# Performance work log

Hardware: AMD Instinct MI355X
Metric: run time of the kernel (lower is better)

## Reference

```python
import jax, jax.numpy as jnp
import numpy as np

N, F, H = 512, 256, 512

def _w(k, i, o):
    return jax.random.normal(k, (i, o), jnp.float32) * (1.0 / np.sqrt(i))

def setup_inputs() -> dict:
    key = jax.random.key(0)
    ks = jax.random.split(key, 12)
    z = lambda n: jnp.zeros((n,), jnp.float32)
    return {
        "node_features": jax.random.normal(ks[0], (N, F), jnp.float32),
        "adjacency": jax.random.uniform(ks[1], (N, N), jnp.float32),
        # GraphConv layers: neighbor linear (wl,bl) and self-loop (ws,bs)
        "gc1_wl": _w(ks[2], F, H), "gc1_bl": z(H), "gc1_ws": _w(ks[3], F, H), "gc1_bs": z(H),
        "gc2_wl": _w(ks[4], H, H), "gc2_bl": z(H), "gc2_ws": _w(ks[5], H, H), "gc2_bs": z(H),
        "gc3_wl": _w(ks[6], H, F), "gc3_bl": z(F), "gc3_ws": _w(ks[7], H, F), "gc3_bs": z(F),
        # edge MLP: Linear(2F,H) -> ReLU -> (dropout=identity, eval) -> Linear(H,H) -> ReLU -> Linear(H,1)
        "mlp_w1": _w(ks[8], 2 * F, H), "mlp_b1": z(H),
        "mlp_w2": _w(ks[9], H, H), "mlp_b2": z(H),
        "mlp_w3": _w(ks[10], H, 1), "mlp_b3": z(1),
    }

def _gconv(x, adj_norm, wl, bl, ws, bs):
    # adj_norm @ Linear(x) + SelfLoop(x)
    return adj_norm @ (x @ wl + bl) + (x @ ws + bs)

def reference(node_features, adjacency,
              gc1_wl, gc1_bl, gc1_ws, gc1_bs,
              gc2_wl, gc2_bl, gc2_ws, gc2_bs,
              gc3_wl, gc3_bl, gc3_ws, gc3_bs,
              mlp_w1, mlp_b1, mlp_w2, mlp_b2, mlp_w3, mlp_b3):
    # row-normalized adjacency (shared across all three layers)
    adj_norm = adjacency / (adjacency.sum(axis=1, keepdims=True) + 1e-8)
    x = jax.nn.relu(_gconv(node_features, adj_norm, gc1_wl, gc1_bl, gc1_ws, gc1_bs))
    x = jax.nn.relu(_gconv(x, adj_norm, gc2_wl, gc2_bl, gc2_ws, gc2_bs))
    emb = _gconv(x, adj_norm, gc3_wl, gc3_bl, gc3_ws, gc3_bs)  # [N, F]
    # vectorized all-pairs (i<j) edge scoring, symmetric scatter
    iu, ju = np.triu_indices(N, k=1)  # static index lists, P = N(N-1)/2
    ef = jnp.concatenate([emb[iu], emb[ju]], axis=-1)  # [P, 2F]
    h = jax.nn.relu(ef @ mlp_w1 + mlp_b1)
    h = jax.nn.relu(h @ mlp_w2 + mlp_b2)
    s = jax.nn.sigmoid((h @ mlp_w3 + mlp_b3)[:, 0])  # [P]
    edge_scores = jnp.zeros((N, N), emb.dtype).at[iu, ju].set(s).at[ju, iu].set(s)
    return emb, edge_scores
```

## Files before the change

### kernel.cpp

```cpp
#include <hip/hip_runtime.h>
#include <hip/hip_bf16.h>


#define NN 512
#define FF 256
#define HH 512

typedef __attribute__((ext_vector_type(8))) short s8v;
typedef __attribute__((ext_vector_type(4))) float f4v;

__device__ __forceinline__ ushort f2bf(float f) {
  unsigned u = __float_as_uint(f);
  unsigned r = (u + 0x7fffu + ((u >> 16) & 1u)) >> 16;
  return (ushort)r;
}

__global__ __launch_bounds__(256)
void prep_kernel(const float* __restrict__ adj, float* __restrict__ adjn,
                 const float* __restrict__ w2, ushort* __restrict__ w2t2) {
  int b = blockIdx.x;
  int tid = threadIdx.x;
  if (b < 512) {
    const float* r = adj + b * NN;
    float a0 = r[tid], a1 = r[tid + 256];
    float s = a0 + a1;
#pragma unroll
    for (int m = 1; m < 64; m <<= 1) s += __shfl_xor(s, m);
    __shared__ float wsum[4];
    if ((tid & 63) == 0) wsum[tid >> 6] = s;
    __syncthreads();
    float inv = 1.f / (wsum[0] + wsum[1] + wsum[2] + wsum[3] + 1e-8f);
    float* o = adjn + b * NN;
    o[tid] = a0 * inv;
    o[tid + 256] = a1 * inv;
  } else {
    int b2 = b - 512;
    int slab = b2 >> 3;
    int col = (b2 & 7) * 64 + (tid >> 2);
    int kq = tid & 3;
    int k0 = slab * 32 + kq * 8;
    ushort tmp[8];
#pragma unroll
    for (int e = 0; e < 8; ++e) tmp[e] = f2bf(w2[(k0 + e) * HH + col]);
    ushort* dst = w2t2 + slab * 16384 + col * 32 + kq * 8;
    *(ushort4*)dst = *(ushort4*)tmp;
    *(ushort4*)(dst + 4) = *(ushort4*)&tmp[4];
  }
}

template <bool RELU>
__global__ __launch_bounds__(256)
void gemm_ts(int M, int N, int K,
             const float* __restrict__ A, int lda,
             const float* __restrict__ B0, const float* __restrict__ B1, int ldb,
             const float* __restrict__ bias0, const float* __restrict__ bias1,
             const float* __restrict__ add0, const float* __restrict__ add1, int ldadd,
             float* __restrict__ C0, float* __restrict__ C1, int ldc)
{
  const float* B = blockIdx.z ? B1 : B0;
  const float* bias = blockIdx.z ? bias1 : bias0;
  const float* add = blockIdx.z ? add1 : add0;
  float* C = blockIdx.z ? C1 : C0;
  const int n0 = blockIdx.x * 64;
  const int m0 = blockIdx.y * 16;
  const int tid = threadIdx.x;
  const int ty = tid >> 4, tx = tid & 15;

  __shared__ float As[32][18];
  __shared__ float Bs[32][68];
  float4 acc = {0.f, 0.f, 0.f, 0.f};

  const int am = tid >> 4;
  const int ak = tid & 15;
  const int bk = tid >> 4;
  const int bn = tid & 15;

  float2 pa = *(const float2*)&A[(m0 + am) * lda + ak * 2];
  float4 pb0 = *(const float4*)&B[bk * ldb + n0 + bn * 4];
  float4 pb1 = *(const float4*)&B[(bk + 16) * ldb + n0 + bn * 4];

  for (int k0 = 0; k0 < K; k0 += 32) {
    As[ak * 2][am] = pa.x;
    As[ak * 2 + 1][am] = pa.y;
    *(float4*)&Bs[bk][bn * 4] = pb0;
    *(float4*)&Bs[bk + 16][bn * 4] = pb1;
    __syncthreads();
    if (k0 + 32 < K) {
      pa = *(const float2*)&A[(m0 + am) * lda + k0 + 32 + ak * 2];
      pb0 = *(const float4*)&B[(k0 + 32 + bk) * ldb + n0 + bn * 4];
      pb1 = *(const float4*)&B[(k0 + 48 + bk) * ldb + n0 + bn * 4];
    }
#pragma unroll
    for (int k = 0; k < 32; ++k) {
      float a = As[k][ty];
      float4 b = *(const float4*)&Bs[k][tx * 4];
      acc.x += a * b.x; acc.y += a * b.y; acc.z += a * b.z; acc.w += a * b.w;
    }
    __syncthreads();
  }

  int m = m0 + ty;
  float4 v = acc;
  if (bias) {
    float4 bv = *(const float4*)&bias[n0 + tx * 4];
    v.x += bv.x; v.y += bv.y; v.z += bv.z; v.w += bv.w;
  }
  if (add) {
    float4 d = *(const float4*)&add[m * ldadd + n0 + tx * 4];
    v.x += d.x; v.y += d.y; v.z += d.z; v.w += d.w;
  }
  if (RELU) {
    v.x = fmaxf(v.x, 0.f); v.y = fmaxf(v.y, 0.f);
    v.z = fmaxf(v.z, 0.f); v.w = fmaxf(v.w, 0.f);
  }
  *(float4*)&C[m * ldc + n0 + tx * 4] = v;
}

__global__ __launch_bounds__(512)
__attribute__((amdgpu_waves_per_eu(2, 2)))
void edge_mlp(const float* __restrict__ Amat, const float* __restrict__ Bmat,
              const ushort* __restrict__ w2t2,
              const float* __restrict__ b2, const float* __restrict__ w3,
              const float* __restrict__ b3,
              float* __restrict__ edges)
{
  __shared__ ushort h1s[2][128 * 128];
  __shared__ float part[8][640];

  const int tb = (int)blockIdx.x;
  int bj = (int)((sqrtf(4.f * tb + 1.f) - 1.f) * 0.5f);
  while (bj * bj + bj > tb) --bj;
  while ((bj + 1) * (bj + 2) <= tb) ++bj;
  const int bi = tb - bj * bj - bj;

  const int tid = threadIdx.x;
  const int wid = tid >> 6;
  const int lane = tid & 63;
  const int l15 = lane & 15;
  const int lg = lane >> 4;

  const f4v zero = {0.f, 0.f, 0.f, 0.f};
  f4v acc[8][4];
#pragma unroll
  for (int mf = 0; mf < 8; ++mf)
#pragma unroll
    for (int nf = 0; nf < 4; ++nf) acc[mf][nf] = zero;

  float4 sa[4], sb[4];
  auto issue_half = [&](int ch, int h) {
#pragma unroll
    for (int q = 0; q < 4; ++q) {
      int fidx = (h * 4 + q) * 512 + tid;
      int p = fidx >> 5;
      int k4 = fidx & 31;
      int i = bi * 8 + (p >> 4);
      int j = bj * 16 + (p & 15);
      sa[q] = *(const float4*)(Amat + i * HH + ch * 128 + k4 * 4);
      sb[q] = *(const float4*)(Bmat + j * HH + ch * 128 + k4 * 4);
    }
  };
  auto write_half = [&](int buf, int h) {
#pragma unroll
    for (int q = 0; q < 4; ++q) {
      int fidx = (h * 4 + q) * 512 + tid;
      int p = fidx >> 5;
      int k4 = fidx & 31;
      ushort4 pk;
      pk.x = f2bf(fmaxf(sa[q].x + sb[q].x, 0.f));
      pk.y = f2bf(fmaxf(sa[q].y + sb[q].y, 0.f));
      pk.z = f2bf(fmaxf(sa[q].z + sb[q].z, 0.f));
      pk.w = f2bf(fmaxf(sa[q].w + sb[q].w, 0.f));
      int off = (p * 256 + k4 * 8) ^ ((p & 7) << 4);
      *(ushort4*)((char*)h1s[buf] + off) = pk;
    }
  };

  issue_half(0, 0); write_half(0, 0);
  issue_half(0, 1); write_half(0, 1);
  __syncthreads();

  const ushort* wbase = w2t2 + wid * 2048 + l15 * 32 + lg * 8;

  s8v nb0, nb1, nb2, nb3;
  nb0 = *(const s8v*)wbase;
  nb1 = *(const s8v*)(wbase + 512);
  nb2 = *(const s8v*)(wbase + 1024);
  nb3 = *(const s8v*)(wbase + 1536);

  auto slab_step = [&](int cur, int slab) {
    s8v cb0 = nb0, cb1 = nb1, cb2 = nb2, cb3 = nb3;
    if (slab < 15) {
      const ushort* wb = wbase + (slab + 1) * 16384;
      nb0 = *(const s8v*)wb;
      nb1 = *(const s8v*)(wb + 512);
      nb2 = *(const s8v*)(wb + 1024);
      nb3 = *(const s8v*)(wb + 1536);
    }
    int ks = slab & 3;
    __builtin_amdgcn_s_barrier();
    __builtin_amdgcn_s_setprio(1);
#pragma unroll
    for (int mf = 0; mf < 8; ++mf) {
      int p = mf * 16 + l15;
      int off = (p * 256 + ks * 64 + lg * 16) ^ ((p & 7) << 4);
      s8v a = *(const s8v*)((const char*)h1s[cur] + off);
      acc[mf][0] = __builtin_amdgcn_mfma_f32_16x16x32_bf16(a, cb0, acc[mf][0], 0, 0, 0);
      acc[mf][1] = __builtin_amdgcn_mfma_f32_16x16x32_bf16(a, cb1, acc[mf][1], 0, 0, 0);
      acc[mf][2] = __builtin_amdgcn_mfma_f32_16x16x32_bf16(a, cb2, acc[mf][2], 0, 0, 0);
      acc[mf][3] = __builtin_amdgcn_mfma_f32_16x16x32_bf16(a, cb3, acc[mf][3], 0, 0, 0);
    }
    __builtin_amdgcn_s_setprio(0);
  };

  for (int ch = 0; ch < 4; ++ch) {
    int cur = ch & 1;
    if (ch < 3) issue_half(ch + 1, 0);
    slab_step(cur, ch * 4 + 0);
    slab_step(cur, ch * 4 + 1);
    if (ch < 3) {
      write_half(cur ^ 1, 0);
      issue_half(ch + 1, 1);
    }
    slab_step(cur, ch * 4 + 2);
    slab_step(cur, ch * 4 + 3);
    if (ch < 3) write_half(cur ^ 1, 1);
    __syncthreads();
  }

  float bb[4], ww[4];
#pragma unroll
  for (int nf = 0; nf < 4; ++nf) {
    int col = wid * 64 + nf * 16 + l15;
    bb[nf] = b2[col];
    ww[nf] = w3[col];
  }
#pragma unroll
  for (int mf = 0; mf < 8; ++mf) {
    float ps[4];
#pragma unroll
    for (int e = 0; e < 4; ++e) {
      ps[e] = fmaxf(acc[mf][0][e] + bb[0], 0.f) * ww[0] +
              fmaxf(acc[mf][1][e] + bb[1], 0.f) * ww[1] +
              fmaxf(acc[mf][2][e] + bb[2], 0.f) * ww[2] +
              fmaxf(acc[mf][3][e] + bb[3], 0.f) * ww[3];
    }
#pragma unroll
    for (int m = 1; m < 16; m <<= 1) {
#pragma unroll
      for (int e = 0; e < 4; ++e) ps[e] += __shfl_xor(ps[e], m);
    }
    if (l15 == 0) {
#pragma unroll
      for (int e = 0; e < 4; ++e)
        part[wid][mf * 16 + lg * 4 + e] = ps[e];
    }
  }
  __syncthreads();
  if (tid < 128) {
    float tot = b3[0];
#pragma unroll
    for (int w = 0; w < 8; ++w) tot += part[w][tid];
    float sg = 1.f / (1.f + expf(-tot));
    int i = bi * 8 + (tid >> 4);
    int j = bj * 16 + (tid & 15);
    if (i < j) {
      edges[i * NN + j] = sg;
      edges[j * NN + i] = sg;
    } else if (i == j) {
      edges[i * NN + i] = 0.f;
    }
  }
}

extern "C" void kernel_launch(void* const* d_in, const int* in_sizes, int n_in,
                              void* d_out, int out_size, void* d_ws, size_t ws_size,
                              hipStream_t stream) {
  const float* node = (const float*)d_in[0];
  const float* adj  = (const float*)d_in[1];
  const float* g1wl = (const float*)d_in[2];
  const float* g1bl = (const float*)d_in[3];
  const float* g1ws = (const float*)d_in[4];
  const float* g1bs = (const float*)d_in[5];
  const float* g2wl = (const float*)d_in[6];
  const float* g2bl = (const float*)d_in[7];
  const float* g2ws = (const float*)d_in[8];
  const float* g2bs = (const float*)d_in[9];
  const float* g3wl = (const float*)d_in[10];
  const float* g3bl = (const float*)d_in[11];
  const float* g3ws = (const float*)d_in[12];
  const float* g3bs = (const float*)d_in[13];
  const float* w1 = (const float*)d_in[14];
  const float* b1 = (const float*)d_in[15];
  const float* w2 = (const float*)d_in[16];
  const float* b2 = (const float*)d_in[17];
  const float* w3 = (const float*)d_in[18];
  const float* b3 = (const float*)d_in[19];

  float* out = (float*)d_out;
  float* emb = out;
  float* edges = out + NN * FF;

  char* wsb = (char*)d_ws;
  float* adjn = (float*)wsb;
  float* Tb   = (float*)(wsb + (1u << 20));
  float* Sb   = (float*)(wsb + (2u << 20));
  float* xa   = (float*)(wsb + (3u << 20));
  float* xb   = (float*)(wsb + (4u << 20));
  ushort* w2t2 = (ushort*)(wsb + (5u << 20));
  float* Amat = Tb;
  float* Bmat = Sb;

  prep_kernel<<<640, 256, 0, stream>>>(adj, adjn, w2, w2t2);

  gemm_ts<false><<<dim3(8, 32, 2), 256, 0, stream>>>(
      NN, HH, FF, node, FF, g1wl, g1ws, HH, g1bl, g1bs,
      nullptr, nullptr, 0, Tb, Sb, HH);
  gemm_ts<true><<<dim3(8, 32, 1), 256, 0, stream>>>(
      NN, HH, NN, adjn, NN, Tb, Tb, HH, nullptr, nullptr,
      Sb, Sb, HH, xa, xa, HH);
  gemm_ts<false><<<dim3(8, 32, 2), 256, 0, stream>>>(
      NN, HH, HH, xa, HH, g2wl, g2ws, HH, g2bl, g2bs,
      nullptr, nullptr, 0, Tb, Sb, HH);
  gemm_ts<true><<<dim3(8, 32, 1), 256, 0, stream>>>(
      NN, HH, NN, adjn, NN, Tb, Tb, HH, nullptr, nullptr,
      Sb, Sb, HH, xb, xb, HH);
  gemm_ts<false><<<dim3(4, 32, 2), 256, 0, stream>>>(
      NN, FF, HH, xb, HH, g3wl, g3ws, FF, g3bl, g3bs,
      nullptr, nullptr, 0, Tb, Sb, FF);
  gemm_ts<false><<<dim3(4, 32, 1), 256, 0, stream>>>(
      NN, FF, NN, adjn, NN, Tb, Tb, FF, nullptr, nullptr,
      Sb, Sb, FF, emb, emb, FF);

  gemm_ts<false><<<dim3(8, 32, 2), 256, 0, stream>>>(
      NN, HH, FF, emb, FF, w1, w1 + FF * HH, HH, b1, nullptr,
      nullptr, nullptr, 0, Amat, Bmat, HH);

  edge_mlp<<<1056, 512, 0, stream>>>(Amat, Bmat, w2t2, b2, w3, b3, edges);
}
```

Measured before the change: 194.2 us.

## Fuse GCN prep and GEMM chain into one cooperative kernel; trim edge_mlp barriers

Replaces the prep kernel and seven separate small GEMM launches with one cooperative kernel of 512 blocks that runs each stage in turn, separated by grid.sync. This removes launch gaps and kernel-boundary drains between many small dependent GEMMs. Separately, edge_mlp drops the per-slab s_barrier and swaps the chunk __syncthreads for an lgkmcnt wait plus s_barrier, and unrolls the chunk loop. Risks are grid-sync overhead, idle blocks in the narrower stages, and possible LDS race hazards from the removed per-slab barriers.

```diff
diff --git a/kernel.cpp b/kernel.cpp
--- a/kernel.cpp
+++ b/kernel.cpp
@@ -1,5 +1,8 @@
 #include <hip/hip_runtime.h>
 #include <hip/hip_bf16.h>
+#include <hip/hip_cooperative_groups.h>
+
+namespace cg = cooperative_groups;
 
 
 #define NN 512
@@ -15,60 +18,17 @@
   return (ushort)r;
 }
 
-__global__ __launch_bounds__(256)
-void prep_kernel(const float* __restrict__ adj, float* __restrict__ adjn,
-                 const float* __restrict__ w2, ushort* __restrict__ w2t2) {
-  int b = blockIdx.x;
-  int tid = threadIdx.x;
-  if (b < 512) {
-    const float* r = adj + b * NN;
-    float a0 = r[tid], a1 = r[tid + 256];
-    float s = a0 + a1;
-#pragma unroll
-    for (int m = 1; m < 64; m <<= 1) s += __shfl_xor(s, m);
-    __shared__ float wsum[4];
-    if ((tid & 63) == 0) wsum[tid >> 6] = s;
-    __syncthreads();
-    float inv = 1.f / (wsum[0] + wsum[1] + wsum[2] + wsum[3] + 1e-8f);
-    float* o = adjn + b * NN;
-    o[tid] = a0 * inv;
-    o[tid + 256] = a1 * inv;
-  } else {
-    int b2 = b - 512;
-    int slab = b2 >> 3;
-    int col = (b2 & 7) * 64 + (tid >> 2);
-    int kq = tid & 3;
-    int k0 = slab * 32 + kq * 8;
-    ushort tmp[8];
-#pragma unroll
-    for (int e = 0; e < 8; ++e) tmp[e] = f2bf(w2[(k0 + e) * HH + col]);
-    ushort* dst = w2t2 + slab * 16384 + col * 32 + kq * 8;
-    *(ushort4*)dst = *(ushort4*)tmp;
-    *(ushort4*)(dst + 4) = *(ushort4*)&tmp[4];
-  }
-}
-
-template <bool RELU>
-__global__ __launch_bounds__(256)
-void gemm_ts(int M, int N, int K,
-             const float* __restrict__ A, int lda,
-             const float* __restrict__ B0, const float* __restrict__ B1, int ldb,
-             const float* __restrict__ bias0, const float* __restrict__ bias1,
-             const float* __restrict__ add0, const float* __restrict__ add1, int ldadd,
-             float* __restrict__ C0, float* __restrict__ C1, int ldc)
+__device__ void tile_gemm(bool relu, int m0, int n0, int K,
+                          const float* __restrict__ A, int lda,
+                          const float* __restrict__ B, int ldb,
+                          const float* __restrict__ bias,
+                          const float* __restrict__ add, int ldadd,
+                          float* __restrict__ C, int ldc, int tid)
 {
-  const float* B = blockIdx.z ? B1 : B0;
-  const float* bias = blockIdx.z ? bias1 : bias0;
-  const float* add = blockIdx.z ? add1 : add0;
-  float* C = blockIdx.z ? C1 : C0;
-  const int n0 = blockIdx.x * 64;
-  const int m0 = blockIdx.y * 16;
-  const int tid = threadIdx.x;
-  const int ty = tid >> 4, tx = tid & 15;
-
   __shared__ float As[32][18];
   __shared__ float Bs[32][68];
   float4 acc = {0.f, 0.f, 0.f, 0.f};
+  const int ty = tid >> 4, tx = tid & 15;
 
   const int am = tid >> 4;
   const int ak = tid & 15;
@@ -109,11 +69,108 @@
     float4 d = *(const float4*)&add[m * ldadd + n0 + tx * 4];
     v.x += d.x; v.y += d.y; v.z += d.z; v.w += d.w;
   }
-  if (RELU) {
+  if (relu) {
     v.x = fmaxf(v.x, 0.f); v.y = fmaxf(v.y, 0.f);
     v.z = fmaxf(v.z, 0.f); v.w = fmaxf(v.w, 0.f);
   }
   *(float4*)&C[m * ldc + n0 + tx * 4] = v;
+}
+
+struct GP {
+  const float *node, *adj, *w2;
+  const float *g1wl, *g1bl, *g1ws, *g1bs;
+  const float *g2wl, *g2bl, *g2ws, *g2bs;
+  const float *g3wl, *g3bl, *g3ws, *g3bs;
+  const float *w1, *b1;
+  float *adjn, *Tb, *Sb, *xa, *xb, *emb, *Amat, *Bmat;
+  ushort *w2t2;
+};
+
+__global__ __launch_bounds__(256)
+void gcn_mega(GP p) {
+  const int b = blockIdx.x;
+  const int tid = threadIdx.x;
+  cg::grid_group grid = cg::this_grid();
+
+  {
+    const float* r = p.adj + b * NN;
+    float a0 = r[tid], a1 = r[tid + 256];
+    float s = a0 + a1;
+#pragma unroll
+    for (int m = 1; m < 64; m <<= 1) s += __shfl_xor(s, m);
+    __shared__ float wsum[4];
+    if ((tid & 63) == 0) wsum[tid >> 6] = s;
+    __syncthreads();
+    float inv = 1.f / (wsum[0] + wsum[1] + wsum[2] + wsum[3] + 1e-8f);
+    float* o = p.adjn + b * NN;
+    o[tid] = a0 * inv;
+    o[tid + 256] = a1 * inv;
+    if (b < 128) {
+      int slab = b >> 3;
+      int col = (b & 7) * 64 + (tid >> 2);
+      int kq = tid & 3;
+      int k0 = slab * 32 + kq * 8;
+      ushort tmp[8];
+#pragma unroll
+      for (int e = 0; e < 8; ++e) tmp[e] = f2bf(p.w2[(k0 + e) * HH + col]);
+      ushort* dst = p.w2t2 + slab * 16384 + col * 32 + kq * 8;
+      *(ushort4*)dst = *(ushort4*)tmp;
+      *(ushort4*)(dst + 4) = *(ushort4*)&tmp[4];
+    }
+  }
+  grid.sync();
+
+  {
+    int z = b >> 8, t = b & 255;
+    int m0 = (t >> 3) * 16, n0 = (t & 7) * 64;
+    tile_gemm(false, m0, n0, FF, p.node, FF, z ? p.g1ws : p.g1wl, HH,
+              z ? p.g1bs : p.g1bl, nullptr, 0, z ? p.Sb : p.Tb, HH, tid);
+  }
+  grid.sync();
+
+  if (b < 256) {
+    int m0 = (b >> 3) * 16, n0 = (b & 7) * 64;
+    tile_gemm(true, m0, n0, NN, p.adjn, NN, p.Tb, HH, nullptr, p.Sb, HH,
+              p.xa, HH, tid);
+  }
+  grid.sync();
+
+  {
+    int z = b >> 8, t = b & 255;
+    int m0 = (t >> 3) * 16, n0 = (t & 7) * 64;
+    tile_gemm(false, m0, n0, HH, p.xa, HH, z ? p.g2ws : p.g2wl, HH,
+              z ? p.g2bs : p.g2bl, nullptr, 0, z ? p.Sb : p.Tb, HH, tid);
+  }
+  grid.sync();
+
+  if (b < 256) {
+    int m0 = (b >> 3) * 16, n0 = (b & 7) * 64;
+    tile_gemm(true, m0, n0, NN, p.adjn, NN, p.Tb, HH, nullptr, p.Sb, HH,
+              p.xb, HH, tid);
+  }
+  grid.sync();
+
+  if (b < 256) {
+    int z = b >> 7, t = b & 127;
+    int m0 = (t >> 2) * 16, n0 = (t & 3) * 64;
+    tile_gemm(false, m0, n0, HH, p.xb, HH, z ? p.g3ws : p.g3wl, FF,
+              z ? p.g3bs : p.g3bl, nullptr, 0, z ? p.Sb : p.Tb, FF, tid);
+  }
+  grid.sync();
+
+  if (b < 128) {
+    int m0 = (b >> 2) * 16, n0 = (b & 3) * 64;
+    tile_gemm(false, m0, n0, NN, p.adjn, NN, p.Tb, FF, nullptr, p.Sb, FF,
+              p.emb, FF, tid);
+  }
+  grid.sync();
+
+  {
+    int z = b >> 8, t = b & 255;
+    int m0 = (t >> 3) * 16, n0 = (t & 7) * 64;
+    tile_gemm(false, m0, n0, FF, p.emb, FF, z ? (p.w1 + FF * HH) : p.w1, HH,
+              z ? nullptr : p.b1, nullptr, 0, z ? p.Bmat : p.Amat, HH, tid);
+  }
 }
 
 __global__ __launch_bounds__(512)
@@ -197,7 +254,6 @@
       nb3 = *(const s8v*)(wb + 1536);
     }
     int ks = slab & 3;
-    __builtin_amdgcn_s_barrier();
     __builtin_amdgcn_s_setprio(1);
 #pragma unroll
     for (int mf = 0; mf < 8; ++mf) {
@@ -212,6 +268,12 @@
     __builtin_amdgcn_s_setprio(0);
   };
 
+  auto chunk_barrier = [] {
+    asm volatile("s_waitcnt lgkmcnt(0)" ::: "memory");
+    __builtin_amdgcn_s_barrier();
+  };
+
+#pragma unroll
   for (int ch = 0; ch < 4; ++ch) {
     int cur = ch & 1;
     if (ch < 3) issue_half(ch + 1, 0);
@@ -224,7 +286,7 @@
     slab_step(cur, ch * 4 + 2);
     slab_step(cur, ch * 4 + 3);
     if (ch < 3) write_half(cur ^ 1, 1);
-    __syncthreads();
+    chunk_barrier();
   }
 
   float bb[4], ww[4];
@@ -310,30 +372,18 @@
   float* Amat = Tb;
   float* Bmat = Sb;
 
-  prep_kernel<<<640, 256, 0, stream>>>(adj, adjn, w2, w2t2);
-
-  gemm_ts<false><<<dim3(8, 32, 2), 256, 0, stream>>>(
-      NN, HH, FF, node, FF, g1wl, g1ws, HH, g1bl, g1bs,
-      nullptr, nullptr, 0, Tb, Sb, HH);
-  gemm_ts<true><<<dim3(8, 32, 1), 256, 0, stream>>>(
-      NN, HH, NN, adjn, NN, Tb, Tb, HH, nullptr, nullptr,
-      Sb, Sb, HH, xa, xa, HH);
-  gemm_ts<false><<<dim3(8, 32, 2), 256, 0, stream>>>(
-      NN, HH, HH, xa, HH, g2wl, g2ws, HH, g2bl, g2bs,
-      nullptr, nullptr, 0, Tb, Sb, HH);
-  gemm_ts<true><<<dim3(8, 32, 1), 256, 0, stream>>>(
-      NN, HH, NN, adjn, NN, Tb, Tb, HH, nullptr, nullptr,
-      Sb, Sb, HH, xb, xb, HH);
-  gemm_ts<false><<<dim3(4, 32, 2), 256, 0, stream>>>(
-      NN, FF, HH, xb, HH, g3wl, g3ws, FF, g3bl, g3bs,
-      nullptr, nullptr, 0, Tb, Sb, FF);
-  gemm_ts<false><<<dim3(4, 32, 1), 256, 0, stream>>>(
-      NN, FF, NN, adjn, NN, Tb, Tb, FF, nullptr, nullptr,
-      Sb, Sb, FF, emb, emb, FF);
-
-  gemm_ts<false><<<dim3(8, 32, 2), 256, 0, stream>>>(
-      NN, HH, FF, emb, FF, w1, w1 + FF * HH, HH, b1, nullptr,
-      nullptr, nullptr, 0, Amat, Bmat, HH);
+  GP P;
+  P.node = node; P.adj = adj; P.w2 = w2;
+  P.g1wl = g1wl; P.g1bl = g1bl; P.g1ws = g1ws; P.g1bs = g1bs;
+  P.g2wl = g2wl; P.g2bl = g2bl; P.g2ws = g2ws; P.g2bs = g2bs;
+  P.g3wl = g3wl; P.g3bl = g3bl; P.g3ws = g3ws; P.g3bs = g3bs;
+  P.w1 = w1; P.b1 = b1;
+  P.adjn = adjn; P.Tb = Tb; P.Sb = Sb; P.xa = xa; P.xb = xb;
+  P.emb = emb; P.Amat = Amat; P.Bmat = Bmat; P.w2t2 = w2t2;
+
+  void* args[] = {&P};
+  hipLaunchCooperativeKernel((const void*)gcn_mega, dim3(512), dim3(256),
+                             args, 0, stream);
 
   edge_mlp<<<1056, 512, 0, stream>>>(Amat, Bmat, w2t2, b2, w3, b3, edges);
 }
```

Measured after the change: 562.4 us. 190% more time.

## Stage unique A/B rows in LDS and build pair activations from shared memory

Applied to the files above, without the earlier changes.

Rather than each thread loading redundant A[i] and B[j] float4 rows from global memory for every pair (8x16 pairs), the block loads only the 24 distinct rows per chunk into a double-buffered LDS staging area, then builds the bf16 h1 tile from LDS. Global traffic and register staging drop sharply. It also replaces per-slab barriers and __syncthreads with fewer lgkmcnt-wait barriers and unrolls the chunk loop. The cost is extra LDS reads and writes and more LDS use, and the barrier placement has to stay correct for the double buffers.

```diff
diff --git a/kernel.cpp b/kernel.cpp
--- a/kernel.cpp
+++ b/kernel.cpp
@@ -125,7 +125,8 @@
               float* __restrict__ edges)
 {
   __shared__ ushort h1s[2][128 * 128];
-  __shared__ float part[8][640];
+  __shared__ float rowsv[2][24][128];
+  __shared__ float part[8][128];
 
   const int tb = (int)blockIdx.x;
   int bj = (int)((sqrtf(4.f * tb + 1.f) - 1.f) * 0.5f);
@@ -146,38 +147,49 @@
 #pragma unroll
     for (int nf = 0; nf < 4; ++nf) acc[mf][nf] = zero;
 
-  float4 sa[4], sb[4];
-  auto issue_half = [&](int ch, int h) {
-#pragma unroll
-    for (int q = 0; q < 4; ++q) {
-      int fidx = (h * 4 + q) * 512 + tid;
+  const int r1 = tid >> 5, kc1 = tid & 31;
+  const int r2 = 16 + (tid >> 5);
+  const float* src1base = (r1 < 8) ? (Amat + (bi * 8 + r1) * HH)
+                                   : (Bmat + (bj * 16 + r1 - 8) * HH);
+  const float* src2base = Bmat + (bj * 16 + r2 - 8) * HH;
+
+  float4 ra, rb;
+  auto issue_rows = [&](int ch) {
+    ra = *(const float4*)(src1base + ch * 128 + kc1 * 4);
+    if (tid < 256) rb = *(const float4*)(src2base + ch * 128 + kc1 * 4);
+  };
+  auto write_rows = [&](int buf) {
+    *(float4*)&rowsv[buf][r1][kc1 * 4] = ra;
+    if (tid < 256) *(float4*)&rowsv[buf][r2][kc1 * 4] = rb;
+  };
+  auto build_h1 = [&](int buf) {
+#pragma unroll
+    for (int q = 0; q < 8; ++q) {
+      int fidx = q * 512 + tid;
       int p = fidx >> 5;
       int k4 = fidx & 31;
-      int i = bi * 8 + (p >> 4);
-      int j = bj * 16 + (p & 15);
-      sa[q] = *(const float4*)(Amat + i * HH + ch * 128 + k4 * 4);
-      sb[q] = *(const float4*)(Bmat + j * HH + ch * 128 + k4 * 4);
-    }
-  };
-  auto write_half = [&](int buf, int h) {
-#pragma unroll
-    for (int q = 0; q < 4; ++q) {
-      int fidx = (h * 4 + q) * 512 + tid;
-      int p = fidx >> 5;
-      int k4 = fidx & 31;
+      float4 av = *(const float4*)&rowsv[buf][p >> 4][k4 * 4];
+      float4 bv = *(const float4*)&rowsv[buf][8 + (p & 15)][k4 * 4];
       ushort4 pk;
-      pk.x = f2bf(fmaxf(sa[q].x + sb[q].x, 0.f));
-      pk.y = f2bf(fmaxf(sa[q].y + sb[q].y, 0.f));
-      pk.z = f2bf(fmaxf(sa[q].z + sb[q].z, 0.f));
-      pk.w = f2bf(fmaxf(sa[q].w + sb[q].w, 0.f));
+      pk.x = f2bf(fmaxf(av.x + bv.x, 0.f));
+      pk.y = f2bf(fmaxf(av.y + bv.y, 0.f));
+      pk.z = f2bf(fmaxf(av.z + bv.z, 0.f));
+      pk.w = f2bf(fmaxf(av.w + bv.w, 0.f));
       int off = (p * 256 + k4 * 8) ^ ((p & 7) << 4);
       *(ushort4*)((char*)h1s[buf] + off) = pk;
     }
   };
 
-  issue_half(0, 0); write_half(0, 0);
-  issue_half(0, 1); write_half(0, 1);
-  __syncthreads();
+  auto lgkm_barrier = [] {
+    asm volatile("s_waitcnt lgkmcnt(0)" ::: "memory");
+    __builtin_amdgcn_s_barrier();
+  };
+
+  issue_rows(0);
+  write_rows(0);
+  lgkm_barrier();
+  build_h1(0);
+  lgkm_barrier();
 
   const ushort* wbase = w2t2 + wid * 2048 + l15 * 32 + lg * 8;
 
@@ -197,7 +209,6 @@
       nb3 = *(const s8v*)(wb + 1536);
     }
     int ks = slab & 3;
-    __builtin_amdgcn_s_barrier();
     __builtin_amdgcn_s_setprio(1);
 #pragma unroll
     for (int mf = 0; mf < 8; ++mf) {
@@ -212,19 +223,20 @@
     __builtin_amdgcn_s_setprio(0);
   };
 
+#pragma unroll
   for (int ch = 0; ch < 4; ++ch) {
     int cur = ch & 1;
-    if (ch < 3) issue_half(ch + 1, 0);
+    if (ch < 3) issue_rows(ch + 1);
     slab_step(cur, ch * 4 + 0);
     slab_step(cur, ch * 4 + 1);
+    if (ch < 3) write_rows(cur ^ 1);
+    slab_step(cur, ch * 4 + 2);
+    if (ch < 3) lgkm_barrier();
+    slab_step(cur, ch * 4 + 3);
     if (ch < 3) {
-      write_half(cur ^ 1, 0);
-      issue_half(ch + 1, 1);
-    }
-    slab_step(cur, ch * 4 + 2);
-    slab_step(cur, ch * 4 + 3);
-    if (ch < 3) write_half(cur ^ 1, 1);
-    __syncthreads();
+      build_h1(cur ^ 1);
+      lgkm_barrier();
+    }
   }
 
   float bb[4], ww[4];
```

After: 188.2 us. -3.1%, faster.
